# Optimization experiments

Hardware: AMD Instinct MI355X
Metric: run time of the kernel (lower is better)

Reference implementation:

```python
import jax, jax.numpy as jnp
import numpy as np

B, S, D, H, P = 2, 1024, 512, 8, 16
DH = D // H
CUT = 15.0
SCALE = DH ** -0.5


def _ln(x, g, b, eps=1e-5):
    m = x.mean(-1, keepdims=True)
    v = ((x - m) ** 2).mean(-1, keepdims=True)
    return (x - m) / jnp.sqrt(v + eps) * g + b


def setup_inputs():
    key = jax.random.key(0)
    ks = jax.random.split(key, 12)
    f32 = jnp.float32
    nrm = lambda k, sh, s: jax.random.normal(k, sh, dtype=f32) * s
    sD = 1.0 / np.sqrt(D)
    HP3 = H * P * 3
    return {
        "x": nrm(ks[0], (B, S, D), 1.0),
        "coords": nrm(ks[1], (B, S, 3), 10.0),  # ~tens of Angstroms so cutoff matters
        "Wq": nrm(ks[2], (D, D), sD),
        "Wk": nrm(ks[3], (D, D), sD),
        "Wv": nrm(ks[4], (D, D), sD),
        "Wqp": nrm(ks[5], (D, HP3), sD), "bqp": jnp.zeros((HP3,), f32),
        "Wkp": nrm(ks[6], (D, HP3), sD), "bkp": jnp.zeros((HP3,), f32),
        "Wvp": nrm(ks[7], (D, HP3), sD), "bvp": jnp.zeros((HP3,), f32),
        "Wd1": nrm(ks[8], (1, 32), 1.0), "bd1": jnp.zeros((32,), f32),
        "Wd2": nrm(ks[9], (32, H), 1.0 / np.sqrt(32)), "bd2": jnp.zeros((H,), f32),
        "Wo": nrm(ks[10], (D + HP3, D), 1.0 / np.sqrt(D + HP3)),
        "bo": jnp.zeros((D,), f32),
        "g1": jnp.ones((D,), f32), "b1": jnp.zeros((D,), f32),
        "g2": jnp.ones((D,), f32), "b2": jnp.zeros((D,), f32),
    }


def reference(x, coords, Wq, Wk, Wv, Wqp, bqp, Wkp, bkp, Wvp, bvp,
              Wd1, bd1, Wd2, bd2, Wo, bo, g1, b1, g2, b2):
    residual = x
    xn = _ln(x, g1, b1)
    q = (xn @ Wq).reshape(B, S, H, DH)
    k = (xn @ Wk).reshape(B, S, H, DH)
    v = (xn @ Wv).reshape(B, S, H, DH)
    ce = coords[:, :, None, None, :]                     # [B,S,1,1,3]
    qp = (xn @ Wqp + bqp).reshape(B, S, H, P, 3) + ce
    kp = (xn @ Wkp + bkp).reshape(B, S, H, P, 3) + ce
    vp = (xn @ Wvp + bvp).reshape(B, S, H, P, 3)
    # pairwise residue distances [B,S,S]
    dist = jnp.linalg.norm(coords[:, :, None, :] - coords[:, None, :, :], axis=-1)
    # small per-pair distance MLP -> per-head bias
    hbias = jax.nn.relu(dist[..., None] @ Wd1 + bd1) @ Wd2 + bd2   # [B,S,S,H]
    dbias = jnp.transpose(hbias, (0, 3, 1, 2))                     # [B,H,S,S]
    spatial = (dist < CUT).astype(x.dtype)[:, None, :, :]          # [B,1,S,S]
    attn = jnp.einsum("bqhd,bkhd->bhqk", q, k) * SCALE
    # -0.5*||qp_i - kp_j||^2 expanded so the [B,H,S,S,P,3] diff tensor is never built
    qn2 = jnp.transpose(jnp.sum(qp * qp, axis=(-2, -1)), (0, 2, 1))  # [B,H,Q]
    kn2 = jnp.transpose(jnp.sum(kp * kp, axis=(-2, -1)), (0, 2, 1))  # [B,H,K]
    pdot = jnp.einsum("bqhpd,bkhpd->bhqk", qp, kp)
    point = -0.5 * (qn2[..., :, None] + kn2[..., None, :] - 2.0 * pdot)
    total = attn + point + dbias
    total = total * spatial + (spatial - 1.0) * 1e9
    w = jax.nn.softmax(total, axis=-1)   # dropout is identity at inference
    af = jnp.einsum("bhqk,bkhd->bqhd", w, v).reshape(B, S, D)
    ap = jnp.einsum("bhqk,bkhpd->bqhpd", w, vp).reshape(B, S, H * P * 3)
    out = jnp.concatenate([af, ap], axis=-1) @ Wo + bo
    out = _ln(residual + out, g2, b2)
    coord_upd = jnp.mean(ap.reshape(B, S, H, P, 3), axis=(2, 3)) * 0.1
    return out, coords + coord_upd
```

## Files before the change

kernel.cpp:

```cpp
#include <hip/hip_runtime.h>
#include <math.h>

#define B_ 2
#define S_ 1024
#define D_ 512
#define H_ 8
#define P_ 16
#define DH_ 64
#define HP3_ 384
#define CONCAT_ 896
#define CUTOFF 15.0f
#define SCALE_ 0.125f
#define QT 32
#define KT 64
#define SQS 68
#define SQPS 52
#define SKS 68
#define SKPS 52
#define SVS 120
#define SWS 68

__device__ __forceinline__ float waveReduceSum(float v) {
#pragma unroll
    for (int o = 32; o; o >>= 1) v += __shfl_down(v, o, 64);
    return v;
}
__device__ __forceinline__ float dot4(float4 a, float4 b, float acc) {
    return fmaf(a.x, b.x, fmaf(a.y, b.y, fmaf(a.z, b.z, fmaf(a.w, b.w, acc))));
}

__global__ __launch_bounds__(256) void ln1_kernel(
    const float* __restrict__ x, const float* __restrict__ g,
    const float* __restrict__ b, float* __restrict__ xn) {
    const int row = blockIdx.x;
    const int t = threadIdx.x;
    const float* xr = x + row * D_;
    float x0 = xr[t], x1 = xr[t + 256];
    __shared__ float red[4];
    float s = waveReduceSum(x0 + x1);
    int lane = t & 63, wid = t >> 6;
    if (lane == 0) red[wid] = s;
    __syncthreads();
    float mean = (red[0] + red[1] + red[2] + red[3]) * (1.0f / D_);
    __syncthreads();
    float d0 = x0 - mean, d1 = x1 - mean;
    float v = waveReduceSum(d0 * d0 + d1 * d1);
    if (lane == 0) red[wid] = v;
    __syncthreads();
    float var = (red[0] + red[1] + red[2] + red[3]) * (1.0f / D_);
    float rs = rsqrtf(var + 1e-5f);
    xn[row * D_ + t]       = d0 * rs * g[t] + b[t];
    xn[row * D_ + t + 256] = d1 * rs * g[t + 256] + b[t + 256];
}

__global__ __launch_bounds__(256) void proj_kernel(
    const float* __restrict__ xn, const float* __restrict__ coords,
    const float* __restrict__ Wq, const float* __restrict__ Wk, const float* __restrict__ Wv,
    const float* __restrict__ Wqp, const float* __restrict__ bqp,
    const float* __restrict__ Wkp, const float* __restrict__ bkp,
    const float* __restrict__ Wvp, const float* __restrict__ bvp,
    float* __restrict__ q, float* __restrict__ k, float* __restrict__ v,
    float* __restrict__ qp, float* __restrict__ kp, float* __restrict__ vp) {
    const int tid = threadIdx.x;
    const int rowBase = blockIdx.y * 64;
    const int colBase = blockIdx.x * 64;

    const float* Wseg; int ldw, segBase, segId;
    if      (colBase < 512)  { Wseg = Wq;  ldw = D_;   segBase = 0;    segId = 0; }
    else if (colBase < 1024) { Wseg = Wk;  ldw = D_;   segBase = 512;  segId = 1; }
    else if (colBase < 1536) { Wseg = Wv;  ldw = D_;   segBase = 1024; segId = 2; }
    else if (colBase < 1920) { Wseg = Wqp; ldw = HP3_; segBase = 1536; segId = 3; }
    else if (colBase < 2304) { Wseg = Wkp; ldw = HP3_; segBase = 1920; segId = 4; }
    else                     { Wseg = Wvp; ldw = HP3_; segBase = 2304; segId = 5; }
    const int segc0 = colBase - segBase;

    __shared__ float As[16][65];
    __shared__ float Bs[16][64];
    const int tx = tid & 15, ty = tid >> 4;

    float acc[4][4];
#pragma unroll
    for (int i = 0; i < 4; i++)
#pragma unroll
        for (int j = 0; j < 4; j++) acc[i][j] = 0.f;

    for (int k0 = 0; k0 < D_; k0 += 16) {
#pragma unroll
        for (int i = 0; i < 4; i++) {
            int e = tid + i * 256;
            int r = e >> 4, kk = e & 15;
            As[kk][r] = xn[(rowBase + r) * D_ + k0 + kk];
            int c = e & 63, kb = e >> 6;
            Bs[kb][c] = Wseg[(k0 + kb) * ldw + segc0 + c];
        }
        __syncthreads();
#pragma unroll
        for (int kk = 0; kk < 16; kk++) {
            float a[4], bb[4];
#pragma unroll
            for (int i = 0; i < 4; i++) a[i] = As[kk][ty * 4 + i];
#pragma unroll
            for (int j = 0; j < 4; j++) bb[j] = Bs[kk][tx * 4 + j];
#pragma unroll
            for (int i = 0; i < 4; i++)
#pragma unroll
                for (int j = 0; j < 4; j++) acc[i][j] = fmaf(a[i], bb[j], acc[i][j]);
        }
        __syncthreads();
    }

#pragma unroll
    for (int i = 0; i < 4; i++) {
        int r = rowBase + ty * 4 + i;
#pragma unroll
        for (int j = 0; j < 4; j++) {
            int lc = segc0 + tx * 4 + j;
            float val = acc[i][j];
            switch (segId) {
                case 0: q[r * D_ + lc] = val; break;
                case 1: k[r * D_ + lc] = val; break;
                case 2: v[r * D_ + lc] = val; break;
                case 3: qp[r * HP3_ + lc] = val + bqp[lc] + coords[r * 3 + lc % 3]; break;
                case 4: kp[r * HP3_ + lc] = val + bkp[lc] + coords[r * 3 + lc % 3]; break;
                case 5: vp[r * HP3_ + lc] = val + bvp[lc]; break;
            }
        }
    }
}

__global__ __launch_bounds__(256) void kn2_kernel(
    const float* __restrict__ kp, float* __restrict__ kn2) {
    int idx = blockIdx.x * 256 + threadIdx.x;
    const float* p = kp + idx * 48;
    float s = 0.f;
#pragma unroll
    for (int i = 0; i < 48; i++) s = fmaf(p[i], p[i], s);
    kn2[idx] = s;
}

__global__ __launch_bounds__(256, 2) void attn_kernel(
    const float* __restrict__ q, const float* __restrict__ k, const float* __restrict__ v,
    const float* __restrict__ qp, const float* __restrict__ kp, const float* __restrict__ vp,
    const float* __restrict__ kn2, const float* __restrict__ coords,
    const float* __restrict__ Wd1, const float* __restrict__ bd1,
    const float* __restrict__ Wd2, const float* __restrict__ bd2,
    float* __restrict__ attn_out) {
    const int qt = blockIdx.x, h = blockIdx.y, b = blockIdx.z;
    const int tid = threadIdx.x;
    const int qpair = tid >> 4;
    const int sub = tid & 15;
    const int q0 = qpair * 2, q1 = q0 + 1;
    const int qbase = qt * QT;

    __shared__ float sQ[QT * SQS];
    __shared__ float sQP[QT * SQPS];
    __shared__ float sKV[7680];
    __shared__ float sWt[QT * SWS];
    __shared__ float sCq[QT * 3], sCk[KT * 3];
    __shared__ float sKn2[KT], sQn2[QT];
    __shared__ float sM[QT], sL[QT], sTm[QT];
    __shared__ float sW1[32], sB1[32], sW2h[32];

    const size_t bq = (size_t)(b * S_ + qbase);
#pragma unroll
    for (int i = 0; i < 2; i++) {
        int f4 = tid + i * 256;
        int r = f4 >> 4, c = f4 & 15;
        *(float4*)&sQ[r * SQS + c * 4] = *(const float4*)(q + (bq + r) * D_ + h * DH_ + c * 4);
    }
    {
        int f4 = tid;
        int r = f4 / 12, c = f4 % 12;
        *(float4*)&sQP[r * SQPS + c * 4] = *(const float4*)(qp + (bq + r) * HP3_ + h * 48 + c * 4);
        if (tid < 128) {
            int f42 = tid + 256;
            int r2 = f42 / 12, c2 = f42 % 12;
            *(float4*)&sQP[r2 * SQPS + c2 * 4] = *(const float4*)(qp + (bq + r2) * HP3_ + h * 48 + c2 * 4);
        }
    }
    if (tid < QT * 3) sCq[tid] = coords[bq * 3 + tid];
    if (tid >= 128 && tid < 160) sW1[tid - 128] = Wd1[tid - 128];
    else if (tid < 192 && tid >= 160) sB1[tid - 160] = bd1[tid - 160];
    else if (tid >= 192 && tid < 224) sW2h[tid - 192] = Wd2[(tid - 192) * H_ + h];
    else if (tid >= 224) { int t2 = tid - 224; sM[t2] = -3.0e38f; sL[t2] = 0.f; }
    __syncthreads();
    if (tid < QT) {
        float s = 0.f;
#pragma unroll
        for (int i = 0; i < 48; i++) s = fmaf(sQP[tid * SQPS + i], sQP[tid * SQPS + i], s);
        sQn2[tid] = s;
    }
    const float bd2h = bd2[h];

    float o0[8] = {0,0,0,0,0,0,0,0}, o1[8] = {0,0,0,0,0,0,0,0};
    const int db = sub * 8;

    for (int kt = 0; kt < S_ / KT; kt++) {
        const size_t bk = (size_t)(b * S_ + kt * KT);
#pragma unroll
        for (int i = 0; i < 4; i++) {
            int f4 = tid + i * 256;
            int r = f4 >> 4, c = f4 & 15;
            *(float4*)&sKV[r * SKS + c * 4] = *(const float4*)(k + (bk + r) * D_ + h * DH_ + c * 4);
        }
#pragma unroll
        for (int i = 0; i < 3; i++) {
            int f4 = tid + i * 256;
            int r = f4 / 12, c = f4 % 12;
            *(float4*)&sKV[4352 + r * SKPS + c * 4] = *(const float4*)(kp + (bk + r) * HP3_ + h * 48 + c * 4);
        }
        if (tid < KT) sKn2[tid] = kn2[(bk + tid) * H_ + h];
        if (tid < KT * 3) sCk[tid] = coords[bk * 3 + tid];
        __syncthreads();

        float ds0[4], ds1[4];
        {
            const float qx0 = sCq[q0*3], qy0 = sCq[q0*3+1], qz0 = sCq[q0*3+2];
            const float qx1 = sCq[q1*3], qy1 = sCq[q1*3+1], qz1 = sCq[q1*3+2];
#pragma unroll
            for (int j = 0; j < 4; j++) {
                int kk = sub + 16 * j;
                float kx = sCk[kk*3], ky = sCk[kk*3+1], kz = sCk[kk*3+2];
                float dx = qx0-kx, dy = qy0-ky, dz = qz0-kz;
                ds0[j] = sqrtf(fmaf(dx,dx,fmaf(dy,dy,dz*dz)));
                dx = qx1-kx; dy = qy1-ky; dz = qz1-kz;
                ds1[j] = sqrtf(fmaf(dx,dx,fmaf(dy,dy,dz*dz)));
            }
        }
        float bias0[4], bias1[4];
#pragma unroll
        for (int j = 0; j < 4; j++) { bias0[j] = bd2h; bias1[j] = bd2h; }
#pragma unroll 4
        for (int jj = 0; jj < 32; jj++) {
            float w1 = sW1[jj], bb = sB1[jj], w2 = sW2h[jj];
#pragma unroll
            for (int j = 0; j < 4; j++) {
                float h0 = fmaf(ds0[j], w1, bb);
                float h1 = fmaf(ds1[j], w1, bb);
                bias0[j] = fmaf(fmaxf(h0, 0.f), w2, bias0[j]);
                bias1[j] = fmaf(fmaxf(h1, 0.f), w2, bias1[j]);
            }
        }
        float d0a[4] = {0,0,0,0}, d1a[4] = {0,0,0,0};
#pragma unroll 4
        for (int d4 = 0; d4 < 16; d4++) {
            float4 a0 = *(const float4*)&sQ[q0 * SQS + d4 * 4];
            float4 a1 = *(const float4*)&sQ[q1 * SQS + d4 * 4];
#pragma unroll
            for (int j = 0; j < 4; j++) {
                float4 bv = *(const float4*)&sKV[(sub + 16 * j) * SKS + d4 * 4];
                d0a[j] = dot4(a0, bv, d0a[j]);
                d1a[j] = dot4(a1, bv, d1a[j]);
            }
        }
#pragma unroll 4
        for (int d4 = 0; d4 < 12; d4++) {
            float4 a0 = *(const float4*)&sQP[q0 * SQPS + d4 * 4];
            float4 a1 = *(const float4*)&sQP[q1 * SQPS + d4 * 4];
#pragma unroll
            for (int j = 0; j < 4; j++) {
                float4 bv = *(const float4*)&sKV[4352 + (sub + 16 * j) * SKPS + d4 * 4];
                bias0[j] = dot4(a0, bv, bias0[j]);
                bias1[j] = dot4(a1, bv, bias1[j]);
            }
        }
        const float qn20 = sQn2[q0], qn21 = sQn2[q1];
        float lg0[4], lg1[4];
#pragma unroll
        for (int j = 0; j < 4; j++) {
            float kn = sKn2[sub + 16 * j];
            float v0 = fmaf(SCALE_, d0a[j], bias0[j]) - 0.5f * (qn20 + kn);
            float v1 = fmaf(SCALE_, d1a[j], bias1[j]) - 0.5f * (qn21 + kn);
            lg0[j] = (ds0[j] < CUTOFF) ? v0 : -1e9f;
            lg1[j] = (ds1[j] < CUTOFF) ? v1 : -1e9f;
        }
        float t0 = fmaxf(fmaxf(lg0[0], lg0[1]), fmaxf(lg0[2], lg0[3]));
        float t1 = fmaxf(fmaxf(lg1[0], lg1[1]), fmaxf(lg1[2], lg1[3]));
#pragma unroll
        for (int off = 1; off < 16; off <<= 1) {
            t0 = fmaxf(t0, __shfl_xor(t0, off, 16));
            t1 = fmaxf(t1, __shfl_xor(t1, off, 16));
        }
        if (sub == 0) { sTm[q0] = t0; sTm[q1] = t1; }
        __syncthreads();
        const float m0o = sM[q0], m1o = sM[q1];
        const float nm0 = fmaxf(m0o, sTm[q0]), nm1 = fmaxf(m1o, sTm[q1]);
        const float sc0 = __expf(m0o - nm0), sc1 = __expf(m1o - nm1);
        float ps0 = 0.f, ps1 = 0.f;
#pragma unroll
        for (int j = 0; j < 4; j++) {
            float w0 = __expf(lg0[j] - nm0);
            float w1 = __expf(lg1[j] - nm1);
            sWt[q0 * SWS + sub + 16 * j] = w0;
            sWt[q1 * SWS + sub + 16 * j] = w1;
            ps0 += w0; ps1 += w1;
        }
#pragma unroll
        for (int off = 1; off < 16; off <<= 1) {
            ps0 += __shfl_xor(ps0, off, 16);
            ps1 += __shfl_xor(ps1, off, 16);
        }
        __syncthreads();
        if (sub == 0) {
            sM[q0] = nm0; sM[q1] = nm1;
            sL[q0] = sL[q0] * sc0 + ps0;
            sL[q1] = sL[q1] * sc1 + ps1;
        }
        {
            int r = tid >> 2, cb = (tid & 3) * 7;
#pragma unroll
            for (int i = 0; i < 7; i++) {
                int c4 = cb + i;
                float4 t;
                if (c4 < 16) t = *(const float4*)(v  + (bk + r) * D_   + h * DH_ + c4 * 4);
                else         t = *(const float4*)(vp + (bk + r) * HP3_ + h * 48  + (c4 - 16) * 4);
                *(float4*)&sKV[r * SVS + c4 * 4] = t;
            }
        }
        __syncthreads();
        if (sub < 14) {
#pragma unroll
            for (int j = 0; j < 8; j++) { o0[j] *= sc0; o1[j] *= sc1; }
            for (int kk4 = 0; kk4 < 16; kk4++) {
                float w0a[4], w1a[4];
                *(float4*)w0a = *(const float4*)&sWt[q0 * SWS + kk4 * 4];
                *(float4*)w1a = *(const float4*)&sWt[q1 * SWS + kk4 * 4];
#pragma unroll
                for (int jj = 0; jj < 4; jj++) {
                    int kk = kk4 * 4 + jj;
                    float4 va = *(const float4*)&sKV[kk * SVS + db];
                    float4 vb = *(const float4*)&sKV[kk * SVS + db + 4];
                    o0[0] = fmaf(w0a[jj], va.x, o0[0]); o0[1] = fmaf(w0a[jj], va.y, o0[1]);
                    o0[2] = fmaf(w0a[jj], va.z, o0[2]); o0[3] = fmaf(w0a[jj], va.w, o0[3]);
                    o0[4] = fmaf(w0a[jj], vb.x, o0[4]); o0[5] = fmaf(w0a[jj], vb.y, o0[5]);
                    o0[6] = fmaf(w0a[jj], vb.z, o0[6]); o0[7] = fmaf(w0a[jj], vb.w, o0[7]);
                    o1[0] = fmaf(w1a[jj], va.x, o1[0]); o1[1] = fmaf(w1a[jj], va.y, o1[1]);
                    o1[2] = fmaf(w1a[jj], va.z, o1[2]); o1[3] = fmaf(w1a[jj], va.w, o1[3]);
                    o1[4] = fmaf(w1a[jj], vb.x, o1[4]); o1[5] = fmaf(w1a[jj], vb.y, o1[5]);
                    o1[6] = fmaf(w1a[jj], vb.z, o1[6]); o1[7] = fmaf(w1a[jj], vb.w, o1[7]);
                }
            }
        }
        __syncthreads();
    }

    if (sub < 14) {
        const float il0 = 1.0f / sL[q0], il1 = 1.0f / sL[q1];
        const int off = (db < 64) ? (h * 64 + db) : (512 + h * 48 + (db - 64));
        float* r0 = attn_out + (size_t)(bq + q0) * CONCAT_ + off;
        float* r1 = attn_out + (size_t)(bq + q1) * CONCAT_ + off;
        float4 w0a, w0b, w1a, w1b;
        w0a.x=o0[0]*il0; w0a.y=o0[1]*il0; w0a.z=o0[2]*il0; w0a.w=o0[3]*il0;
        w0b.x=o0[4]*il0; w0b.y=o0[5]*il0; w0b.z=o0[6]*il0; w0b.w=o0[7]*il0;
        w1a.x=o1[0]*il1; w1a.y=o1[1]*il1; w1a.z=o1[2]*il1; w1a.w=o1[3]*il1;
        w1b.x=o1[4]*il1; w1b.y=o1[5]*il1; w1b.z=o1[6]*il1; w1b.w=o1[7]*il1;
        *(float4*)r0 = w0a; *(float4*)(r0 + 4) = w0b;
        *(float4*)r1 = w1a; *(float4*)(r1 + 4) = w1b;
    }
}

__global__ __launch_bounds__(256) void ogemm_kernel(
    const float* __restrict__ aout, const float* __restrict__ x,
    const float* __restrict__ Wo, const float* __restrict__ bo,
    float* __restrict__ yres) {
    const int tid = threadIdx.x;
    const int rowBase = blockIdx.y * 64;
    const int colBase = blockIdx.x * 64;

    __shared__ float As[16][65];
    __shared__ float Bs[16][64];
    const int tx = tid & 15, ty = tid >> 4;

    float acc[4][4];
#pragma unroll
    for (int i = 0; i < 4; i++)
#pragma unroll
        for (int j = 0; j < 4; j++) acc[i][j] = 0.f;

    for (int k0 = 0; k0 < CONCAT_; k0 += 16) {
#pragma unroll
        for (int i = 0; i < 4; i++) {
            int e = tid + i * 256;
            int r = e >> 4, kk = e & 15;
            As[kk][r] = aout[(size_t)(rowBase + r) * CONCAT_ + k0 + kk];
            int c = e & 63, kb = e >> 6;
            Bs[kb][c] = Wo[(k0 + kb) * D_ + colBase + c];
        }
        __syncthreads();
#pragma unroll
        for (int kk = 0; kk < 16; kk++) {
            float a[4], bb[4];
#pragma unroll
            for (int i = 0; i < 4; i++) a[i] = As[kk][ty * 4 + i];
#pragma unroll
            for (int j = 0; j < 4; j++) bb[j] = Bs[kk][tx * 4 + j];
#pragma unroll
            for (int i = 0; i < 4; i++)
#pragma unroll
                for (int j = 0; j < 4; j++) acc[i][j] = fmaf(a[i], bb[j], acc[i][j]);
        }
        __syncthreads();
    }

#pragma unroll
    for (int i = 0; i < 4; i++) {
        int r = rowBase + ty * 4 + i;
#pragma unroll
        for (int j = 0; j < 4; j++) {
            int lc = colBase + tx * 4 + j;
            yres[(size_t)r * D_ + lc] = acc[i][j] + bo[lc] + x[(size_t)r * D_ + lc];
        }
    }
}

__global__ __launch_bounds__(64) void coord_kernel(
    const float* __restrict__ aout, const float* __restrict__ coords,
    float* __restrict__ coords_out) {
    const int row = blockIdx.x;
    const int t = threadIdx.x;
    const float* ap = aout + (size_t)row * CONCAT_ + 512;
    float c0 = ap[t * 3]     + ap[(t + 64) * 3];
    float c1 = ap[t * 3 + 1] + ap[(t + 64) * 3 + 1];
    float c2 = ap[t * 3 + 2] + ap[(t + 64) * 3 + 2];
#pragma unroll
    for (int o = 32; o; o >>= 1) {
        c0 += __shfl_down(c0, o, 64);
        c1 += __shfl_down(c1, o, 64);
        c2 += __shfl_down(c2, o, 64);
    }
    if (t == 0) {
        coords_out[row * 3 + 0] = coords[row * 3 + 0] + c0 * (0.1f / 128.f);
        coords_out[row * 3 + 1] = coords[row * 3 + 1] + c1 * (0.1f / 128.f);
        coords_out[row * 3 + 2] = coords[row * 3 + 2] + c2 * (0.1f / 128.f);
    }
}

extern "C" void kernel_launch(void* const* d_in, const int* in_sizes, int n_in,
                              void* d_out, int out_size, void* d_ws, size_t ws_size,
                              hipStream_t stream) {
    const float* x      = (const float*)d_in[0];
    const float* coords = (const float*)d_in[1];
    const float* Wq     = (const float*)d_in[2];
    const float* Wk     = (const float*)d_in[3];
    const float* Wv     = (const float*)d_in[4];
    const float* Wqp    = (const float*)d_in[5];
    const float* bqp    = (const float*)d_in[6];
    const float* Wkp    = (const float*)d_in[7];
    const float* bkp    = (const float*)d_in[8];
    const float* Wvp    = (const float*)d_in[9];
    const float* bvp    = (const float*)d_in[10];
    const float* Wd1    = (const float*)d_in[11];
    const float* bd1    = (const float*)d_in[12];
    const float* Wd2    = (const float*)d_in[13];
    const float* bd2    = (const float*)d_in[14];
    const float* Wo     = (const float*)d_in[15];
    const float* bo     = (const float*)d_in[16];
    const float* g1     = (const float*)d_in[17];
    const float* b1     = (const float*)d_in[18];
    const float* g2     = (const float*)d_in[19];
    const float* b2     = (const float*)d_in[20];

    float* out        = (float*)d_out;
    float* coords_out = (float*)d_out + (size_t)B_ * S_ * D_;

    float* ws = (float*)d_ws;
    const size_t NROW = (size_t)B_ * S_;
    float* xn   = ws;
    float* q    = xn   + NROW * D_;
    float* k    = q    + NROW * D_;
    float* v    = k    + NROW * D_;
    float* qp   = v    + NROW * D_;
    float* kp   = qp   + NROW * HP3_;
    float* vp   = kp   + NROW * HP3_;
    float* kn2  = vp   + NROW * HP3_;
    float* aout = kn2  + NROW * H_;

    ln1_kernel<<<NROW, 256, 0, stream>>>(x, g1, b1, xn);

    dim3 pgrid(2688 / 64, 2048 / 64);
    proj_kernel<<<pgrid, 256, 0, stream>>>(xn, coords, Wq, Wk, Wv,
                                           Wqp, bqp, Wkp, bkp, Wvp, bvp,
                                           q, k, v, qp, kp, vp);

    kn2_kernel<<<(NROW * H_) / 256, 256, 0, stream>>>(kp, kn2);

    dim3 agrid(S_ / QT, H_, B_);
    attn_kernel<<<agrid, 256, 0, stream>>>(q, k, v, qp, kp, vp, kn2, coords,
                                           Wd1, bd1, Wd2, bd2, aout);

    float* yres = xn;
    dim3 ogrid(D_ / 64, 2048 / 64);
    ogemm_kernel<<<ogrid, 256, 0, stream>>>(aout, x, Wo, bo, yres);

    ln1_kernel<<<NROW, 256, 0, stream>>>(yres, g2, b2, out);

    coord_kernel<<<NROW, 64, 0, stream>>>(aout, coords, coords_out);
}
```

Baseline: 492.9 us.

## Store K and V tiles as bf16 in LDS, keep softmax stats in registers

```diff
diff --git a/kernel.cpp b/kernel.cpp
--- a/kernel.cpp
+++ b/kernel.cpp
@@ -15,9 +15,9 @@
 #define KT 64
 #define SQS 68
 #define SQPS 52
-#define SKS 68
+#define SKBS 36
 #define SKPS 52
-#define SVS 120
+#define SVBS 60
 #define SWS 68
 
 __device__ __forceinline__ float waveReduceSum(float v) {
@@ -27,6 +27,17 @@
 }
 __device__ __forceinline__ float dot4(float4 a, float4 b, float acc) {
     return fmaf(a.x, b.x, fmaf(a.y, b.y, fmaf(a.z, b.z, fmaf(a.w, b.w, acc))));
+}
+__device__ __forceinline__ unsigned rne16(float x) {
+    unsigned u = __float_as_uint(x);
+    return (u + 0x7fffu + ((u >> 16) & 1u)) >> 16;
+}
+__device__ __forceinline__ uint2 pk4(float4 t) {
+    return make_uint2(rne16(t.x) | (rne16(t.y) << 16), rne16(t.z) | (rne16(t.w) << 16));
+}
+__device__ __forceinline__ void unp2(unsigned u, float& a, float& b) {
+    a = __uint_as_float(u << 16);
+    b = __uint_as_float(u & 0xffff0000u);
 }
 
 __global__ __launch_bounds__(256) void ln1_kernel(
@@ -152,13 +163,13 @@
     const int q0 = qpair * 2, q1 = q0 + 1;
     const int qbase = qt * QT;
 
-    __shared__ float sQ[QT * SQS];
-    __shared__ float sQP[QT * SQPS];
-    __shared__ float sKV[7680];
-    __shared__ float sWt[QT * SWS];
-    __shared__ float sCq[QT * 3], sCk[KT * 3];
-    __shared__ float sKn2[KT], sQn2[QT];
-    __shared__ float sM[QT], sL[QT], sTm[QT];
+    __shared__ __align__(16) float    sQ[QT * SQS];
+    __shared__ __align__(16) float    sQP[QT * SQPS];
+    __shared__ __align__(16) unsigned sKb[KT * SKBS];
+    __shared__ __align__(16) float    sKP[KT * SKPS];
+    __shared__ __align__(16) unsigned sVb[KT * SVBS];
+    __shared__ __align__(16) float    sWt[QT * SWS];
+    __shared__ float sCq[QT * 3], sCk[KT * 3], sKn2[KT];
     __shared__ float sW1[32], sB1[32], sW2h[32];
 
     const size_t bq = (size_t)(b * S_ + qbase);
@@ -169,8 +180,7 @@
         *(float4*)&sQ[r * SQS + c * 4] = *(const float4*)(q + (bq + r) * D_ + h * DH_ + c * 4);
     }
     {
-        int f4 = tid;
-        int r = f4 / 12, c = f4 % 12;
+        int r = tid / 12, c = tid % 12;
         *(float4*)&sQP[r * SQPS + c * 4] = *(const float4*)(qp + (bq + r) * HP3_ + h * 48 + c * 4);
         if (tid < 128) {
             int f42 = tid + 256;
@@ -180,20 +190,24 @@
     }
     if (tid < QT * 3) sCq[tid] = coords[bq * 3 + tid];
     if (tid >= 128 && tid < 160) sW1[tid - 128] = Wd1[tid - 128];
-    else if (tid < 192 && tid >= 160) sB1[tid - 160] = bd1[tid - 160];
+    else if (tid >= 160 && tid < 192) sB1[tid - 160] = bd1[tid - 160];
     else if (tid >= 192 && tid < 224) sW2h[tid - 192] = Wd2[(tid - 192) * H_ + h];
-    else if (tid >= 224) { int t2 = tid - 224; sM[t2] = -3.0e38f; sL[t2] = 0.f; }
     __syncthreads();
-    if (tid < QT) {
-        float s = 0.f;
-#pragma unroll
-        for (int i = 0; i < 48; i++) s = fmaf(sQP[tid * SQPS + i], sQP[tid * SQPS + i], s);
-        sQn2[tid] = s;
-    }
+
+    float qn20 = 0.f, qn21 = 0.f;
+#pragma unroll
+    for (int i = 0; i < 12; i++) {
+        float4 t0 = *(const float4*)&sQP[q0 * SQPS + i * 4];
+        qn20 = dot4(t0, t0, qn20);
+        float4 t1 = *(const float4*)&sQP[q1 * SQPS + i * 4];
+        qn21 = dot4(t1, t1, qn21);
+    }
+    const float cqx0 = sCq[q0*3], cqy0 = sCq[q0*3+1], cqz0 = sCq[q0*3+2];
+    const float cqx1 = sCq[q1*3], cqy1 = sCq[q1*3+1], cqz1 = sCq[q1*3+2];
     const float bd2h = bd2[h];
 
+    float m0 = -3.0e38f, m1 = -3.0e38f, l0 = 0.f, l1 = 0.f;
     float o0[8] = {0,0,0,0,0,0,0,0}, o1[8] = {0,0,0,0,0,0,0,0};
-    const int db = sub * 8;
 
     for (int kt = 0; kt < S_ / KT; kt++) {
         const size_t bk = (size_t)(b * S_ + kt * KT);
@@ -201,31 +215,37 @@
         for (int i = 0; i < 4; i++) {
             int f4 = tid + i * 256;
             int r = f4 >> 4, c = f4 & 15;
-            *(float4*)&sKV[r * SKS + c * 4] = *(const float4*)(k + (bk + r) * D_ + h * DH_ + c * 4);
+            float4 t = *(const float4*)(k + (bk + r) * D_ + h * DH_ + c * 4);
+            *(uint2*)&sKb[r * SKBS + c * 2] = pk4(t);
         }
 #pragma unroll
         for (int i = 0; i < 3; i++) {
             int f4 = tid + i * 256;
             int r = f4 / 12, c = f4 % 12;
-            *(float4*)&sKV[4352 + r * SKPS + c * 4] = *(const float4*)(kp + (bk + r) * HP3_ + h * 48 + c * 4);
+            *(float4*)&sKP[r * SKPS + c * 4] = *(const float4*)(kp + (bk + r) * HP3_ + h * 48 + c * 4);
+        }
+#pragma unroll
+        for (int i = 0; i < 7; i++) {
+            int f4 = tid + i * 256;
+            int r = f4 / 28, c4 = f4 % 28;
+            float4 t;
+            if (c4 < 16) t = *(const float4*)(v  + (bk + r) * D_   + h * DH_ + c4 * 4);
+            else         t = *(const float4*)(vp + (bk + r) * HP3_ + h * 48  + (c4 - 16) * 4);
+            *(uint2*)&sVb[r * SVBS + c4 * 2] = pk4(t);
         }
         if (tid < KT) sKn2[tid] = kn2[(bk + tid) * H_ + h];
         if (tid < KT * 3) sCk[tid] = coords[bk * 3 + tid];
         __syncthreads();
 
         float ds0[4], ds1[4];
-        {
-            const float qx0 = sCq[q0*3], qy0 = sCq[q0*3+1], qz0 = sCq[q0*3+2];
-            const float qx1 = sCq[q1*3], qy1 = sCq[q1*3+1], qz1 = sCq[q1*3+2];
-#pragma unroll
-            for (int j = 0; j < 4; j++) {
-                int kk = sub + 16 * j;
-                float kx = sCk[kk*3], ky = sCk[kk*3+1], kz = sCk[kk*3+2];
-                float dx = qx0-kx, dy = qy0-ky, dz = qz0-kz;
-                ds0[j] = sqrtf(fmaf(dx,dx,fmaf(dy,dy,dz*dz)));
-                dx = qx1-kx; dy = qy1-ky; dz = qz1-kz;
-                ds1[j] = sqrtf(fmaf(dx,dx,fmaf(dy,dy,dz*dz)));
-            }
+#pragma unroll
+        for (int j = 0; j < 4; j++) {
+            int kk = sub + 16 * j;
+            float kx = sCk[kk*3], ky = sCk[kk*3+1], kz = sCk[kk*3+2];
+            float dx = cqx0-kx, dy = cqy0-ky, dz = cqz0-kz;
+            ds0[j] = sqrtf(fmaf(dx,dx,fmaf(dy,dy,dz*dz)));
+            dx = cqx1-kx; dy = cqy1-ky; dz = cqz1-kz;
+            ds1[j] = sqrtf(fmaf(dx,dx,fmaf(dy,dy,dz*dz)));
         }
         float bias0[4], bias1[4];
 #pragma unroll
@@ -242,15 +262,21 @@
             }
         }
         float d0a[4] = {0,0,0,0}, d1a[4] = {0,0,0,0};
-#pragma unroll 4
-        for (int d4 = 0; d4 < 16; d4++) {
-            float4 a0 = *(const float4*)&sQ[q0 * SQS + d4 * 4];
-            float4 a1 = *(const float4*)&sQ[q1 * SQS + d4 * 4];
+#pragma unroll 2
+        for (int d8 = 0; d8 < 8; d8++) {
+            float4 a0l = *(const float4*)&sQ[q0 * SQS + d8 * 8];
+            float4 a0h = *(const float4*)&sQ[q0 * SQS + d8 * 8 + 4];
+            float4 a1l = *(const float4*)&sQ[q1 * SQS + d8 * 8];
+            float4 a1h = *(const float4*)&sQ[q1 * SQS + d8 * 8 + 4];
 #pragma unroll
             for (int j = 0; j < 4; j++) {
-                float4 bv = *(const float4*)&sKV[(sub + 16 * j) * SKS + d4 * 4];
-                d0a[j] = dot4(a0, bv, d0a[j]);
-                d1a[j] = dot4(a1, bv, d1a[j]);
+                uint4 kw = *(const uint4*)&sKb[(sub + 16 * j) * SKBS + d8 * 4];
+                float k0,k1,k2,k3,k4,k5,k6,k7;
+                unp2(kw.x,k0,k1); unp2(kw.y,k2,k3); unp2(kw.z,k4,k5); unp2(kw.w,k6,k7);
+                d0a[j] = fmaf(a0l.x,k0,fmaf(a0l.y,k1,fmaf(a0l.z,k2,fmaf(a0l.w,k3,d0a[j]))));
+                d0a[j] = fmaf(a0h.x,k4,fmaf(a0h.y,k5,fmaf(a0h.z,k6,fmaf(a0h.w,k7,d0a[j]))));
+                d1a[j] = fmaf(a1l.x,k0,fmaf(a1l.y,k1,fmaf(a1l.z,k2,fmaf(a1l.w,k3,d1a[j]))));
+                d1a[j] = fmaf(a1h.x,k4,fmaf(a1h.y,k5,fmaf(a1h.z,k6,fmaf(a1h.w,k7,d1a[j]))));
             }
         }
 #pragma unroll 4
@@ -259,12 +285,11 @@
             float4 a1 = *(const float4*)&sQP[q1 * SQPS + d4 * 4];
 #pragma unroll
             for (int j = 0; j < 4; j++) {
-                float4 bv = *(const float4*)&sKV[4352 + (sub + 16 * j) * SKPS + d4 * 4];
+                float4 bv = *(const float4*)&sKP[(sub + 16 * j) * SKPS + d4 * 4];
                 bias0[j] = dot4(a0, bv, bias0[j]);
                 bias1[j] = dot4(a1, bv, bias1[j]);
             }
         }
-        const float qn20 = sQn2[q0], qn21 = sQn2[q1];
         float lg0[4], lg1[4];
 #pragma unroll
         for (int j = 0; j < 4; j++) {
@@ -281,11 +306,9 @@
             t0 = fmaxf(t0, __shfl_xor(t0, off, 16));
             t1 = fmaxf(t1, __shfl_xor(t1, off, 16));
         }
-        if (sub == 0) { sTm[q0] = t0; sTm[q1] = t1; }
-        __syncthreads();
-        const float m0o = sM[q0], m1o = sM[q1];
-        const float nm0 = fmaxf(m0o, sTm[q0]), nm1 = fmaxf(m1o, sTm[q1]);
-        const float sc0 = __expf(m0o - nm0), sc1 = __expf(m1o - nm1);
+        const float nm0 = fmaxf(m0, t0), nm1 = fmaxf(m1, t1);
+        const float sc0 = __expf(m0 - nm0), sc1 = __expf(m1 - nm1);
+        m0 = nm0; m1 = nm1;
         float ps0 = 0.f, ps1 = 0.f;
 #pragma unroll
         for (int j = 0; j < 4; j++) {
@@ -300,27 +323,12 @@
             ps0 += __shfl_xor(ps0, off, 16);
             ps1 += __shfl_xor(ps1, off, 16);
         }
-        __syncthreads();
-        if (sub == 0) {
-            sM[q0] = nm0; sM[q1] = nm1;
-            sL[q0] = sL[q0] * sc0 + ps0;
-            sL[q1] = sL[q1] * sc1 + ps1;
-        }
-        {
-            int r = tid >> 2, cb = (tid & 3) * 7;
-#pragma unroll
-            for (int i = 0; i < 7; i++) {
-                int c4 = cb + i;
-                float4 t;
-                if (c4 < 16) t = *(const float4*)(v  + (bk + r) * D_   + h * DH_ + c4 * 4);
-                else         t = *(const float4*)(vp + (bk + r) * HP3_ + h * 48  + (c4 - 16) * 4);
-                *(float4*)&sKV[r * SVS + c4 * 4] = t;
-            }
-        }
-        __syncthreads();
+        l0 = l0 * sc0 + ps0;
+        l1 = l1 * sc1 + ps1;
+
+#pragma unroll
+        for (int j = 0; j < 8; j++) { o0[j] *= sc0; o1[j] *= sc1; }
         if (sub < 14) {
-#pragma unroll
-            for (int j = 0; j < 8; j++) { o0[j] *= sc0; o1[j] *= sc1; }
             for (int kk4 = 0; kk4 < 16; kk4++) {
                 float w0a[4], w1a[4];
                 *(float4*)w0a = *(const float4*)&sWt[q0 * SWS + kk4 * 4];
@@ -328,16 +336,18 @@
 #pragma unroll
                 for (int jj = 0; jj < 4; jj++) {
                     int kk = kk4 * 4 + jj;
-                    float4 va = *(const float4*)&sKV[kk * SVS + db];
-                    float4 vb = *(const float4*)&sKV[kk * SVS + db + 4];
-                    o0[0] = fmaf(w0a[jj], va.x, o0[0]); o0[1] = fmaf(w0a[jj], va.y, o0[1]);
-                    o0[2] = fmaf(w0a[jj], va.z, o0[2]); o0[3] = fmaf(w0a[jj], va.w, o0[3]);
-                    o0[4] = fmaf(w0a[jj], vb.x, o0[4]); o0[5] = fmaf(w0a[jj], vb.y, o0[5]);
-                    o0[6] = fmaf(w0a[jj], vb.z, o0[6]); o0[7] = fmaf(w0a[jj], vb.w, o0[7]);
-                    o1[0] = fmaf(w1a[jj], va.x, o1[0]); o1[1] = fmaf(w1a[jj], va.y, o1[1]);
-                    o1[2] = fmaf(w1a[jj], va.z, o1[2]); o1[3] = fmaf(w1a[jj], va.w, o1[3]);
-                    o1[4] = fmaf(w1a[jj], vb.x, o1[4]); o1[5] = fmaf(w1a[jj], vb.y, o1[5]);
-                    o1[6] = fmaf(w1a[jj], vb.z, o1[6]); o1[7] = fmaf(w1a[jj], vb.w, o1[7]);
+                    uint4 vw = *(const uint4*)&sVb[kk * SVBS + sub * 4];
+                    float v0,v1,v2,v3,v4,v5,v6,v7;
+                    unp2(vw.x,v0,v1); unp2(vw.y,v2,v3); unp2(vw.z,v4,v5); unp2(vw.w,v6,v7);
+                    float w0 = w0a[jj], w1 = w1a[jj];
+                    o0[0]=fmaf(w0,v0,o0[0]); o0[1]=fmaf(w0,v1,o0[1]);
+                    o0[2]=fmaf(w0,v2,o0[2]); o0[3]=fmaf(w0,v3,o0[3]);
+                    o0[4]=fmaf(w0,v4,o0[4]); o0[5]=fmaf(w0,v5,o0[5]);
+                    o0[6]=fmaf(w0,v6,o0[6]); o0[7]=fmaf(w0,v7,o0[7]);
+                    o1[0]=fmaf(w1,v0,o1[0]); o1[1]=fmaf(w1,v1,o1[1]);
+                    o1[2]=fmaf(w1,v2,o1[2]); o1[3]=fmaf(w1,v3,o1[3]);
+                    o1[4]=fmaf(w1,v4,o1[4]); o1[5]=fmaf(w1,v5,o1[5]);
+                    o1[6]=fmaf(w1,v6,o1[6]); o1[7]=fmaf(w1,v7,o1[7]);
                 }
             }
         }
@@ -345,7 +355,8 @@
     }
 
     if (sub < 14) {
-        const float il0 = 1.0f / sL[q0], il1 = 1.0f / sL[q1];
+        const int db = sub * 8;
+        const float il0 = 1.0f / l0, il1 = 1.0f / l1;
         const int off = (db < 64) ? (h * 64 + db) : (512 + h * 48 + (db - 64));
         float* r0 = attn_out + (size_t)(bq + q0) * CONCAT_ + off;
         float* r1 = attn_out + (size_t)(bq + q1) * CONCAT_ + off;
```

Measured after the change: 537.6 us. 1.09x slower.
